# Kernel tuning notes

Hardware: AMD Instinct MI355X
Metric: run time of the kernel (lower is better)

## Reference

```python
import jax, jax.numpy as jnp
import numpy as np

EPS = 1e-8

def _conv(x, w, b=None):
    # NCHW conv, stride 1, SAME padding (k=3, pad=1)
    y = jax.lax.conv_general_dilated(x, w, (1, 1), 'SAME',
                                     dimension_numbers=('NCHW', 'OIHW', 'NCHW'))
    if b is not None:
        y = y + b[None, :, None, None]
    return y

def setup_inputs() -> dict:
    key = jax.random.key(0)
    ks = jax.random.split(key, 6)
    B, C, H, W = 512, 1024, 8, 8
    return {
        'x': jax.random.normal(ks[0], (B, C, H, W), jnp.float32),
        'w1_1': jax.random.normal(ks[1], (1, 1, 3, 3), jnp.float32) * 0.1,
        'w5': jax.random.normal(ks[2], (4, 2, 3, 3), jnp.float32) * 0.1,
        'b5': jax.random.normal(ks[3], (4,), jnp.float32) * 0.1,
        'w6': jax.random.normal(ks[4], (1, 4, 3, 3), jnp.float32) * 0.1,
        'b6': jax.random.normal(ks[5], (1,), jnp.float32) * 0.1,
    }

def reference(x, w1_1, w5, b5, w6, b6):
    B, C, H, W = x.shape  # H == W == 8 by module construction
    m = jnp.max(x, axis=1, keepdims=True)  # [B,1,H,W] channel max
    # 2x2 non-overlapping windows, torch unfold layout -> [B,1,(H/2)*(W/2),4]
    win = m.reshape(B, 1, H // 2, 2, W // 2, 2)
    win = win.transpose(0, 1, 2, 4, 3, 5).reshape(B, 1, (H // 2) * (W // 2), 4)
    # probabilistic pooling: clean inf/nan/negatives, sample per window
    winc = jnp.where(jnp.isinf(win) | jnp.isnan(win) | (win < 0), EPS, win)
    skey = jax.random.key(1)
    idx = jax.random.categorical(skey, winc, axis=-1)  # softmax(winc) multinomial
    mo2 = jnp.take_along_axis(winc, idx[..., None], axis=-1)[..., 0]
    mo2 = mo2.reshape(B, 1, H // 2, W // 2)
    # adaptive max/avg pool (4,4) on 8x8 == 2x2 pooling, reuse windows
    mo3 = win.max(axis=-1).reshape(B, 1, H // 2, W // 2)
    ao4 = win.mean(axis=-1).reshape(B, 1, H // 2, W // 2)
    out2 = 0.1 * mo2 + 0.6 * mo3 + 0.3 * ao4
    out2 = _conv(out2, w1_1)  # bias-free 1->1 conv
    out2 = jax.image.resize(out2, (B, 1, H, W), method='bilinear')  # align_corners=False
    out1 = jnp.concatenate([m, out2], axis=1)  # [B,2,H,W]
    gate = jax.nn.sigmoid(_conv(jax.nn.relu(_conv(out1, w5, b5)), w6, b6))  # [B,1,H,W]
    return jax.nn.relu(x * gate)
```

## Files before the change

### kernel.cpp

```cpp
#include <hip/hip_runtime.h>
#include <math.h>

#define C_DIM 1024
#define HW 64
#define F4B 16384
#define EPSV 1e-8f
#define TINYF 1.17549435e-38f

typedef float f32x4_t __attribute__((ext_vector_type(4)));

__device__ __forceinline__ void threefry2x32_01(unsigned x0, unsigned x1,
                                                unsigned& o0, unsigned& o1) {
    const unsigned ks0 = 0u, ks1 = 1u, ks2 = 0x1BD11BDBu;
    x0 += ks0; x1 += ks1;
#define TF_R(r) { x0 += x1; x1 = (x1 << (r)) | (x1 >> (32 - (r))); x1 ^= x0; }
    TF_R(13) TF_R(15) TF_R(26) TF_R(6)
    x0 += ks1; x1 += ks2 + 1u;
    TF_R(17) TF_R(29) TF_R(16) TF_R(24)
    x0 += ks2; x1 += ks0 + 2u;
    TF_R(13) TF_R(15) TF_R(26) TF_R(6)
    x0 += ks0; x1 += ks1 + 3u;
    TF_R(17) TF_R(29) TF_R(16) TF_R(24)
    x0 += ks1; x1 += ks2 + 4u;
    TF_R(13) TF_R(15) TF_R(26) TF_R(6)
    x0 += ks2; x1 += ks0 + 5u;
#undef TF_R
    o0 = x0; o1 = x1;
}

__device__ __forceinline__ unsigned jax_random_bits(unsigned n) {
    unsigned o0, o1;
    threefry2x32_01(0u, n, o0, o1);
    return o0 ^ o1;
}

__device__ __forceinline__ float gumbel01(unsigned n) {
    unsigned bits = jax_random_bits(n);
    float f = __uint_as_float(0x3F800000u | (bits >> 9)) - 1.0f;
    float u = fmaxf(TINYF, f + TINYF);
    return -logf(-logf(u));
}

__device__ __forceinline__ bool bad_val(float v) {
    return ((__float_as_uint(v) & 0x7F800000u) == 0x7F800000u) || (v < 0.0f);
}

__global__ __launch_bounds__(256) void sa_maxpart_kernel(
    const float* __restrict__ x,
    float* __restrict__ part)
{
    const int bid = blockIdx.x;
    const int t = threadIdx.x;
    const int b = bid >> 2, q = bid & 3;

    const float4* __restrict__ xq =
        (const float4*)x + (size_t)b * F4B + (size_t)q * 4096;

    float4 pm = make_float4(-INFINITY, -INFINITY, -INFINITY, -INFINITY);
#pragma unroll
    for (int i = 0; i < 16; ++i) {
        float4 v = xq[t + 256 * i];
        pm.x = fmaxf(pm.x, v.x); pm.y = fmaxf(pm.y, v.y);
        pm.z = fmaxf(pm.z, v.z); pm.w = fmaxf(pm.w, v.w);
    }
#pragma unroll
    for (int off = 16; off <= 32; off <<= 1) {
        pm.x = fmaxf(pm.x, __shfl_xor(pm.x, off, 64));
        pm.y = fmaxf(pm.y, __shfl_xor(pm.y, off, 64));
        pm.z = fmaxf(pm.z, __shfl_xor(pm.z, off, 64));
        pm.w = fmaxf(pm.w, __shfl_xor(pm.w, off, 64));
    }
    __shared__ float4 red[4 * 16];
    const int wv = t >> 6, lane = t & 63;
    if (lane < 16) red[wv * 16 + lane] = pm;
    __syncthreads();
    if (t < 16) {
        float4 a = red[t];
#pragma unroll
        for (int w = 1; w < 4; ++w) {
            float4 o = red[w * 16 + t];
            a.x = fmaxf(a.x, o.x); a.y = fmaxf(a.y, o.y);
            a.z = fmaxf(a.z, o.z); a.w = fmaxf(a.w, o.w);
        }
        float* dst = part + ((size_t)b * 4 + q) * 64 + t * 4;
        dst[0] = a.x; dst[1] = a.y; dst[2] = a.z; dst[3] = a.w;
    }
}

__global__ __launch_bounds__(64) void sa_middle_kernel(
    const float* __restrict__ part,
    const float* __restrict__ w11,
    const float* __restrict__ w5,
    const float* __restrict__ b5,
    const float* __restrict__ w6,
    const float* __restrict__ b6,
    float* __restrict__ gate)
{
    const int b = blockIdx.x;
    const int t = threadIdx.x;

    __shared__ float sm[64], sa16[16], sb16[16], so2[64], shid[4 * 64];

    const float* pb = part + (size_t)b * 256;
    float m = fmaxf(fmaxf(pb[t], pb[64 + t]), fmaxf(pb[128 + t], pb[192 + t]));
    sm[t] = m;
    const float sgum = gumbel01((unsigned)(b * 64 + t));
    __builtin_amdgcn_wave_barrier();

    {
        int w = t >> 2, j = t & 3;
        int hh = 2 * (w >> 2) + (j >> 1), ww = 2 * (w & 3) + (j & 1);
        float v = sm[hh * 8 + ww];
        float wc = bad_val(v) ? EPSV : v;
        float s = wc + sgum;
        int bi = j;
        float bwc = wc;
        float mx = v;
        float ssum = v;
#pragma unroll
        for (int mk = 1; mk <= 2; mk <<= 1) {
            float s2   = __shfl_xor(s, mk, 64);
            int   bi2  = __shfl_xor(bi, mk, 64);
            float bwc2 = __shfl_xor(bwc, mk, 64);
            float mx2  = __shfl_xor(mx, mk, 64);
            float ss2  = __shfl_xor(ssum, mk, 64);
            bool take = (s2 > s) || (s2 == s && bi2 < bi);
            if (take) { s = s2; bi = bi2; bwc = bwc2; }
            mx = fmaxf(mx, mx2);
            ssum += ss2;
        }
        if (j == 0) sa16[w] = 0.1f * bwc + 0.6f * mx + 0.3f * (ssum * 0.25f);
    }
    __builtin_amdgcn_wave_barrier();

    if (t < 16) {
        int i = t >> 2, j = t & 3;
        float acc = 0.0f;
#pragma unroll
        for (int dy = -1; dy <= 1; ++dy) {
            int yy = i + dy;
            if (yy < 0 || yy > 3) continue;
#pragma unroll
            for (int dx = -1; dx <= 1; ++dx) {
                int xx = j + dx;
                if (xx < 0 || xx > 3) continue;
                acc += sa16[yy * 4 + xx] * w11[(dy + 1) * 3 + (dx + 1)];
            }
        }
        sb16[t] = acc;
    }
    __builtin_amdgcn_wave_barrier();

    {
        int y = t >> 3, xx2 = t & 7;
        float sy = (y + 0.5f) * 0.5f - 0.5f;
        float sx = (xx2 + 0.5f) * 0.5f - 0.5f;
        float fy = fminf(fmaxf(sy, 0.0f), 3.0f);
        float fx = fminf(fmaxf(sx, 0.0f), 3.0f);
        int iy0 = (int)floorf(fy); int iy1 = min(iy0 + 1, 3); float ry = fy - (float)iy0;
        int ix0 = (int)floorf(fx); int ix1 = min(ix0 + 1, 3); float rx = fx - (float)ix0;
        float v00 = sb16[iy0 * 4 + ix0], v01 = sb16[iy0 * 4 + ix1];
        float v10 = sb16[iy1 * 4 + ix0], v11 = sb16[iy1 * 4 + ix1];
        float top = v00 * (1.0f - rx) + v01 * rx;
        float bot = v10 * (1.0f - rx) + v11 * rx;
        so2[t] = top * (1.0f - ry) + bot * ry;
    }
    __builtin_amdgcn_wave_barrier();

    {
        int y = t >> 3, x2 = t & 7;
        float a0 = b5[0], a1 = b5[1], a2 = b5[2], a3 = b5[3];
#pragma unroll
        for (int dy = -1; dy <= 1; ++dy) {
            int yy = y + dy;
            if (yy < 0 || yy > 7) continue;
#pragma unroll
            for (int dx = -1; dx <= 1; ++dx) {
                int xx = x2 + dx;
                if (xx < 0 || xx > 7) continue;
                float i0 = sm[yy * 8 + xx];
                float i1 = so2[yy * 8 + xx];
                int kk = (dy + 1) * 3 + (dx + 1);
                a0 += i0 * w5[0 * 18 + kk] + i1 * w5[0 * 18 + 9 + kk];
                a1 += i0 * w5[1 * 18 + kk] + i1 * w5[1 * 18 + 9 + kk];
                a2 += i0 * w5[2 * 18 + kk] + i1 * w5[2 * 18 + 9 + kk];
                a3 += i0 * w5[3 * 18 + kk] + i1 * w5[3 * 18 + 9 + kk];
            }
        }
        shid[0 * 64 + t] = fmaxf(a0, 0.0f);
        shid[1 * 64 + t] = fmaxf(a1, 0.0f);
        shid[2 * 64 + t] = fmaxf(a2, 0.0f);
        shid[3 * 64 + t] = fmaxf(a3, 0.0f);
    }
    __builtin_amdgcn_wave_barrier();

    {
        int y = t >> 3, x2 = t & 7;
        float acc = b6[0];
#pragma unroll
        for (int dy = -1; dy <= 1; ++dy) {
            int yy = y + dy;
            if (yy < 0 || yy > 7) continue;
#pragma unroll
            for (int dx = -1; dx <= 1; ++dx) {
                int xx = x2 + dx;
                if (xx < 0 || xx > 7) continue;
                int kk = (dy + 1) * 3 + (dx + 1);
                int p = yy * 8 + xx;
                acc += shid[0 * 64 + p] * w6[0 + kk]
                     + shid[1 * 64 + p] * w6[9 + kk]
                     + shid[2 * 64 + p] * w6[18 + kk]
                     + shid[3 * 64 + p] * w6[27 + kk];
            }
        }
        gate[(size_t)b * 64 + t] = 1.0f / (1.0f + expf(-acc));
    }
}

__global__ __launch_bounds__(256) void sa_apply_kernel(
    const float* __restrict__ x,
    const float* __restrict__ gate,
    float* __restrict__ out)
{
    const int bid = blockIdx.x;
    const int t = threadIdx.x;
    const int b = bid >> 2;
    const size_t base = (size_t)bid * 4096;

    const float4* __restrict__ x4 = (const float4*)x;
    float4* __restrict__ o4 = (float4*)out;

    const float4 gv = ((const float4*)(gate + (size_t)b * 64))[t & 15];

#pragma unroll
    for (int i = 0; i < 16; ++i) {
        size_t idx = base + t + 256 * i;
        float4 v = x4[idx];
        f32x4_t o;
        o.x = fmaxf(v.x * gv.x, 0.0f);
        o.y = fmaxf(v.y * gv.y, 0.0f);
        o.z = fmaxf(v.z * gv.z, 0.0f);
        o.w = fmaxf(v.w * gv.w, 0.0f);
        __builtin_nontemporal_store(o, (f32x4_t*)&o4[idx]);
    }
}

extern "C" void kernel_launch(void* const* d_in, const int* in_sizes, int n_in,
                              void* d_out, int out_size, void* d_ws, size_t ws_size,
                              hipStream_t stream) {
    const float* x   = (const float*)d_in[0];
    const float* w11 = (const float*)d_in[1];
    const float* w5  = (const float*)d_in[2];
    const float* b5  = (const float*)d_in[3];
    const float* w6  = (const float*)d_in[4];
    const float* b6  = (const float*)d_in[5];
    float* out  = (float*)d_out;

    int B = in_sizes[0] / (C_DIM * HW);
    float* gate = (float*)d_ws;
    float* part = (float*)d_ws + (size_t)B * 64;

    sa_maxpart_kernel<<<dim3(B * 4), dim3(256), 0, stream>>>(x, part);
    sa_middle_kernel<<<dim3(B), dim3(64), 0, stream>>>(part, w11, w5, b5, w6, b6, gate);
    sa_apply_kernel<<<dim3(B * 4), dim3(256), 0, stream>>>(x, gate, out);
}
```

Before: 262.4 us.

## Fuse three kernels into one cooperative kernel with grid-wide syncs

Replaces the separate max-reduction, middle gate, and apply launches with one cooperative kernel of 2*B blocks. Each block handles two channel quarters, and grid.sync separates the three phases. This is meant to remove launch gaps between kernels and to let the second pass over x hit in cache. The cost is two grid-wide barriers, a cap on grid size from the cooperative-launch occupancy limit, and only B of the 2B blocks doing the tiny middle work.

```diff
diff --git a/kernel.cpp b/kernel.cpp
--- a/kernel.cpp
+++ b/kernel.cpp
@@ -1,5 +1,8 @@
 #include <hip/hip_runtime.h>
+#include <hip/hip_cooperative_groups.h>
 #include <math.h>
+
+namespace cg = cooperative_groups;
 
 #define C_DIM 1024
 #define HW 64
@@ -45,203 +48,202 @@
     return ((__float_as_uint(v) & 0x7F800000u) == 0x7F800000u) || (v < 0.0f);
 }
 
-__global__ __launch_bounds__(256) void sa_maxpart_kernel(
+__global__ __launch_bounds__(256, 4) void sa_coop_kernel(
     const float* __restrict__ x,
-    float* __restrict__ part)
-{
-    const int bid = blockIdx.x;
-    const int t = threadIdx.x;
-    const int b = bid >> 2, q = bid & 3;
-
-    const float4* __restrict__ xq =
-        (const float4*)x + (size_t)b * F4B + (size_t)q * 4096;
-
-    float4 pm = make_float4(-INFINITY, -INFINITY, -INFINITY, -INFINITY);
-#pragma unroll
-    for (int i = 0; i < 16; ++i) {
-        float4 v = xq[t + 256 * i];
-        pm.x = fmaxf(pm.x, v.x); pm.y = fmaxf(pm.y, v.y);
-        pm.z = fmaxf(pm.z, v.z); pm.w = fmaxf(pm.w, v.w);
-    }
-#pragma unroll
-    for (int off = 16; off <= 32; off <<= 1) {
-        pm.x = fmaxf(pm.x, __shfl_xor(pm.x, off, 64));
-        pm.y = fmaxf(pm.y, __shfl_xor(pm.y, off, 64));
-        pm.z = fmaxf(pm.z, __shfl_xor(pm.z, off, 64));
-        pm.w = fmaxf(pm.w, __shfl_xor(pm.w, off, 64));
-    }
-    __shared__ float4 red[4 * 16];
-    const int wv = t >> 6, lane = t & 63;
-    if (lane < 16) red[wv * 16 + lane] = pm;
-    __syncthreads();
-    if (t < 16) {
-        float4 a = red[t];
-#pragma unroll
-        for (int w = 1; w < 4; ++w) {
-            float4 o = red[w * 16 + t];
-            a.x = fmaxf(a.x, o.x); a.y = fmaxf(a.y, o.y);
-            a.z = fmaxf(a.z, o.z); a.w = fmaxf(a.w, o.w);
-        }
-        float* dst = part + ((size_t)b * 4 + q) * 64 + t * 4;
-        dst[0] = a.x; dst[1] = a.y; dst[2] = a.z; dst[3] = a.w;
-    }
-}
-
-__global__ __launch_bounds__(64) void sa_middle_kernel(
-    const float* __restrict__ part,
     const float* __restrict__ w11,
     const float* __restrict__ w5,
     const float* __restrict__ b5,
     const float* __restrict__ w6,
     const float* __restrict__ b6,
-    float* __restrict__ gate)
+    float* __restrict__ out,
+    float* __restrict__ part,
+    float* __restrict__ gate,
+    int B)
 {
-    const int b = blockIdx.x;
-    const int t = threadIdx.x;
-
-    __shared__ float sm[64], sa16[16], sb16[16], so2[64], shid[4 * 64];
-
-    const float* pb = part + (size_t)b * 256;
-    float m = fmaxf(fmaxf(pb[t], pb[64 + t]), fmaxf(pb[128 + t], pb[192 + t]));
-    sm[t] = m;
-    const float sgum = gumbel01((unsigned)(b * 64 + t));
-    __builtin_amdgcn_wave_barrier();
-
-    {
-        int w = t >> 2, j = t & 3;
-        int hh = 2 * (w >> 2) + (j >> 1), ww = 2 * (w & 3) + (j & 1);
-        float v = sm[hh * 8 + ww];
-        float wc = bad_val(v) ? EPSV : v;
-        float s = wc + sgum;
-        int bi = j;
-        float bwc = wc;
-        float mx = v;
-        float ssum = v;
-#pragma unroll
-        for (int mk = 1; mk <= 2; mk <<= 1) {
-            float s2   = __shfl_xor(s, mk, 64);
-            int   bi2  = __shfl_xor(bi, mk, 64);
-            float bwc2 = __shfl_xor(bwc, mk, 64);
-            float mx2  = __shfl_xor(mx, mk, 64);
-            float ss2  = __shfl_xor(ssum, mk, 64);
-            bool take = (s2 > s) || (s2 == s && bi2 < bi);
-            if (take) { s = s2; bi = bi2; bwc = bwc2; }
-            mx = fmaxf(mx, mx2);
-            ssum += ss2;
-        }
-        if (j == 0) sa16[w] = 0.1f * bwc + 0.6f * mx + 0.3f * (ssum * 0.25f);
-    }
-    __builtin_amdgcn_wave_barrier();
-
-    if (t < 16) {
-        int i = t >> 2, j = t & 3;
-        float acc = 0.0f;
-#pragma unroll
-        for (int dy = -1; dy <= 1; ++dy) {
-            int yy = i + dy;
-            if (yy < 0 || yy > 3) continue;
-#pragma unroll
-            for (int dx = -1; dx <= 1; ++dx) {
-                int xx = j + dx;
-                if (xx < 0 || xx > 3) continue;
-                acc += sa16[yy * 4 + xx] * w11[(dy + 1) * 3 + (dx + 1)];
-            }
-        }
-        sb16[t] = acc;
-    }
-    __builtin_amdgcn_wave_barrier();
-
-    {
-        int y = t >> 3, xx2 = t & 7;
-        float sy = (y + 0.5f) * 0.5f - 0.5f;
-        float sx = (xx2 + 0.5f) * 0.5f - 0.5f;
-        float fy = fminf(fmaxf(sy, 0.0f), 3.0f);
-        float fx = fminf(fmaxf(sx, 0.0f), 3.0f);
-        int iy0 = (int)floorf(fy); int iy1 = min(iy0 + 1, 3); float ry = fy - (float)iy0;
-        int ix0 = (int)floorf(fx); int ix1 = min(ix0 + 1, 3); float rx = fx - (float)ix0;
-        float v00 = sb16[iy0 * 4 + ix0], v01 = sb16[iy0 * 4 + ix1];
-        float v10 = sb16[iy1 * 4 + ix0], v11 = sb16[iy1 * 4 + ix1];
-        float top = v00 * (1.0f - rx) + v01 * rx;
-        float bot = v10 * (1.0f - rx) + v11 * rx;
-        so2[t] = top * (1.0f - ry) + bot * ry;
-    }
-    __builtin_amdgcn_wave_barrier();
-
-    {
-        int y = t >> 3, x2 = t & 7;
-        float a0 = b5[0], a1 = b5[1], a2 = b5[2], a3 = b5[3];
-#pragma unroll
-        for (int dy = -1; dy <= 1; ++dy) {
-            int yy = y + dy;
-            if (yy < 0 || yy > 7) continue;
-#pragma unroll
-            for (int dx = -1; dx <= 1; ++dx) {
-                int xx = x2 + dx;
-                if (xx < 0 || xx > 7) continue;
-                float i0 = sm[yy * 8 + xx];
-                float i1 = so2[yy * 8 + xx];
-                int kk = (dy + 1) * 3 + (dx + 1);
-                a0 += i0 * w5[0 * 18 + kk] + i1 * w5[0 * 18 + 9 + kk];
-                a1 += i0 * w5[1 * 18 + kk] + i1 * w5[1 * 18 + 9 + kk];
-                a2 += i0 * w5[2 * 18 + kk] + i1 * w5[2 * 18 + 9 + kk];
-                a3 += i0 * w5[3 * 18 + kk] + i1 * w5[3 * 18 + 9 + kk];
-            }
-        }
-        shid[0 * 64 + t] = fmaxf(a0, 0.0f);
-        shid[1 * 64 + t] = fmaxf(a1, 0.0f);
-        shid[2 * 64 + t] = fmaxf(a2, 0.0f);
-        shid[3 * 64 + t] = fmaxf(a3, 0.0f);
-    }
-    __builtin_amdgcn_wave_barrier();
-
-    {
-        int y = t >> 3, x2 = t & 7;
-        float acc = b6[0];
-#pragma unroll
-        for (int dy = -1; dy <= 1; ++dy) {
-            int yy = y + dy;
-            if (yy < 0 || yy > 7) continue;
-#pragma unroll
-            for (int dx = -1; dx <= 1; ++dx) {
-                int xx = x2 + dx;
-                if (xx < 0 || xx > 7) continue;
-                int kk = (dy + 1) * 3 + (dx + 1);
-                int p = yy * 8 + xx;
-                acc += shid[0 * 64 + p] * w6[0 + kk]
-                     + shid[1 * 64 + p] * w6[9 + kk]
-                     + shid[2 * 64 + p] * w6[18 + kk]
-                     + shid[3 * 64 + p] * w6[27 + kk];
-            }
-        }
-        gate[(size_t)b * 64 + t] = 1.0f / (1.0f + expf(-acc));
-    }
-}
-
-__global__ __launch_bounds__(256) void sa_apply_kernel(
-    const float* __restrict__ x,
-    const float* __restrict__ gate,
-    float* __restrict__ out)
-{
+    cg::grid_group grid = cg::this_grid();
     const int bid = blockIdx.x;
     const int t = threadIdx.x;
-    const int b = bid >> 2;
-    const size_t base = (size_t)bid * 4096;
-
+    const int nblk = gridDim.x;
     const float4* __restrict__ x4 = (const float4*)x;
     float4* __restrict__ o4 = (float4*)out;
 
-    const float4 gv = ((const float4*)(gate + (size_t)b * 64))[t & 15];
-
-#pragma unroll
-    for (int i = 0; i < 16; ++i) {
-        size_t idx = base + t + 256 * i;
-        float4 v = x4[idx];
-        f32x4_t o;
-        o.x = fmaxf(v.x * gv.x, 0.0f);
-        o.y = fmaxf(v.y * gv.y, 0.0f);
-        o.z = fmaxf(v.z * gv.z, 0.0f);
-        o.w = fmaxf(v.w * gv.w, 0.0f);
-        __builtin_nontemporal_store(o, (f32x4_t*)&o4[idx]);
+    __shared__ float4 red[2][4 * 16];
+    __shared__ float sm[64], sa16[16], sb16[16], so2[64], shid[4 * 64];
+
+#pragma unroll
+    for (int r = 0; r < 2; ++r) {
+        const int qb = bid + r * nblk;
+        const size_t base = (size_t)qb * 4096;
+        float4 pm = make_float4(-INFINITY, -INFINITY, -INFINITY, -INFINITY);
+#pragma unroll
+        for (int i = 0; i < 16; ++i) {
+            float4 v = x4[base + t + 256 * i];
+            pm.x = fmaxf(pm.x, v.x); pm.y = fmaxf(pm.y, v.y);
+            pm.z = fmaxf(pm.z, v.z); pm.w = fmaxf(pm.w, v.w);
+        }
+#pragma unroll
+        for (int off = 16; off <= 32; off <<= 1) {
+            pm.x = fmaxf(pm.x, __shfl_xor(pm.x, off, 64));
+            pm.y = fmaxf(pm.y, __shfl_xor(pm.y, off, 64));
+            pm.z = fmaxf(pm.z, __shfl_xor(pm.z, off, 64));
+            pm.w = fmaxf(pm.w, __shfl_xor(pm.w, off, 64));
+        }
+        const int wv = t >> 6, lane = t & 63;
+        if (lane < 16) red[r][wv * 16 + lane] = pm;
+    }
+    __syncthreads();
+    if (t < 16) {
+#pragma unroll
+        for (int r = 0; r < 2; ++r) {
+            float4 a = red[r][t];
+#pragma unroll
+            for (int w = 1; w < 4; ++w) {
+                float4 o = red[r][w * 16 + t];
+                a.x = fmaxf(a.x, o.x); a.y = fmaxf(a.y, o.y);
+                a.z = fmaxf(a.z, o.z); a.w = fmaxf(a.w, o.w);
+            }
+            float* dst = part + (size_t)(bid + r * nblk) * 64 + t * 4;
+            dst[0] = a.x; dst[1] = a.y; dst[2] = a.z; dst[3] = a.w;
+        }
+    }
+    grid.sync();
+
+    if (bid < B && t < 64) {
+        const int b = bid;
+        const float* pb = part + (size_t)b * 256;
+        float m = fmaxf(fmaxf(pb[t], pb[64 + t]), fmaxf(pb[128 + t], pb[192 + t]));
+        sm[t] = m;
+        const float sgum = gumbel01((unsigned)(b * 64 + t));
+        __builtin_amdgcn_wave_barrier();
+
+        {
+            int w = t >> 2, j = t & 3;
+            int hh = 2 * (w >> 2) + (j >> 1), ww = 2 * (w & 3) + (j & 1);
+            float v = sm[hh * 8 + ww];
+            float wc = bad_val(v) ? EPSV : v;
+            float s = wc + sgum;
+            int bi = j;
+            float bwc = wc;
+            float mx = v;
+            float ssum = v;
+#pragma unroll
+            for (int mk = 1; mk <= 2; mk <<= 1) {
+                float s2   = __shfl_xor(s, mk, 64);
+                int   bi2  = __shfl_xor(bi, mk, 64);
+                float bwc2 = __shfl_xor(bwc, mk, 64);
+                float mx2  = __shfl_xor(mx, mk, 64);
+                float ss2  = __shfl_xor(ssum, mk, 64);
+                bool take = (s2 > s) || (s2 == s && bi2 < bi);
+                if (take) { s = s2; bi = bi2; bwc = bwc2; }
+                mx = fmaxf(mx, mx2);
+                ssum += ss2;
+            }
+            if (j == 0) sa16[w] = 0.1f * bwc + 0.6f * mx + 0.3f * (ssum * 0.25f);
+        }
+        __builtin_amdgcn_wave_barrier();
+
+        if (t < 16) {
+            int i = t >> 2, j = t & 3;
+            float acc = 0.0f;
+#pragma unroll
+            for (int dy = -1; dy <= 1; ++dy) {
+                int yy = i + dy;
+                if (yy < 0 || yy > 3) continue;
+#pragma unroll
+                for (int dx = -1; dx <= 1; ++dx) {
+                    int xx = j + dx;
+                    if (xx < 0 || xx > 3) continue;
+                    acc += sa16[yy * 4 + xx] * w11[(dy + 1) * 3 + (dx + 1)];
+                }
+            }
+            sb16[t] = acc;
+        }
+        __builtin_amdgcn_wave_barrier();
+
+        {
+            int y = t >> 3, xx2 = t & 7;
+            float sy = (y + 0.5f) * 0.5f - 0.5f;
+            float sx = (xx2 + 0.5f) * 0.5f - 0.5f;
+            float fy = fminf(fmaxf(sy, 0.0f), 3.0f);
+            float fx = fminf(fmaxf(sx, 0.0f), 3.0f);
+            int iy0 = (int)floorf(fy); int iy1 = min(iy0 + 1, 3); float ry = fy - (float)iy0;
+            int ix0 = (int)floorf(fx); int ix1 = min(ix0 + 1, 3); float rx = fx - (float)ix0;
+            float v00 = sb16[iy0 * 4 + ix0], v01 = sb16[iy0 * 4 + ix1];
+            float v10 = sb16[iy1 * 4 + ix0], v11 = sb16[iy1 * 4 + ix1];
+            float top = v00 * (1.0f - rx) + v01 * rx;
+            float bot = v10 * (1.0f - rx) + v11 * rx;
+            so2[t] = top * (1.0f - ry) + bot * ry;
+        }
+        __builtin_amdgcn_wave_barrier();
+
+        {
+            int y = t >> 3, x2 = t & 7;
+            float a0 = b5[0], a1 = b5[1], a2 = b5[2], a3 = b5[3];
+#pragma unroll
+            for (int dy = -1; dy <= 1; ++dy) {
+                int yy = y + dy;
+                if (yy < 0 || yy > 7) continue;
+#pragma unroll
+                for (int dx = -1; dx <= 1; ++dx) {
+                    int xx = x2 + dx;
+                    if (xx < 0 || xx > 7) continue;
+                    float i0 = sm[yy * 8 + xx];
+                    float i1 = so2[yy * 8 + xx];
+                    int kk = (dy + 1) * 3 + (dx + 1);
+                    a0 += i0 * w5[0 * 18 + kk] + i1 * w5[0 * 18 + 9 + kk];
+                    a1 += i0 * w5[1 * 18 + kk] + i1 * w5[1 * 18 + 9 + kk];
+                    a2 += i0 * w5[2 * 18 + kk] + i1 * w5[2 * 18 + 9 + kk];
+                    a3 += i0 * w5[3 * 18 + kk] + i1 * w5[3 * 18 + 9 + kk];
+                }
+            }
+            shid[0 * 64 + t] = fmaxf(a0, 0.0f);
+            shid[1 * 64 + t] = fmaxf(a1, 0.0f);
+            shid[2 * 64 + t] = fmaxf(a2, 0.0f);
+            shid[3 * 64 + t] = fmaxf(a3, 0.0f);
+        }
+        __builtin_amdgcn_wave_barrier();
+
+        {
+            int y = t >> 3, x2 = t & 7;
+            float acc = b6[0];
+#pragma unroll
+            for (int dy = -1; dy <= 1; ++dy) {
+                int yy = y + dy;
+                if (yy < 0 || yy > 7) continue;
+#pragma unroll
+                for (int dx = -1; dx <= 1; ++dx) {
+                    int xx = x2 + dx;
+                    if (xx < 0 || xx > 7) continue;
+                    int kk = (dy + 1) * 3 + (dx + 1);
+                    int p = yy * 8 + xx;
+                    acc += shid[0 * 64 + p] * w6[0 + kk]
+                         + shid[1 * 64 + p] * w6[9 + kk]
+                         + shid[2 * 64 + p] * w6[18 + kk]
+                         + shid[3 * 64 + p] * w6[27 + kk];
+                }
+            }
+            gate[(size_t)b * 64 + t] = 1.0f / (1.0f + expf(-acc));
+        }
+    }
+    grid.sync();
+
+#pragma unroll
+    for (int r = 0; r < 2; ++r) {
+        const int qb = bid + r * nblk;
+        const int b = qb >> 2;
+        const size_t base = (size_t)qb * 4096;
+        const float4 gv = ((const float4*)(gate + (size_t)b * 64))[t & 15];
+#pragma unroll
+        for (int i = 0; i < 16; ++i) {
+            size_t idx = base + t + 256 * i;
+            float4 v = x4[idx];
+            f32x4_t o;
+            o.x = fmaxf(v.x * gv.x, 0.0f);
+            o.y = fmaxf(v.y * gv.y, 0.0f);
+            o.z = fmaxf(v.z * gv.z, 0.0f);
+            o.w = fmaxf(v.w * gv.w, 0.0f);
+            __builtin_nontemporal_store(o, (f32x4_t*)&o4[idx]);
+        }
     }
 }
 
@@ -260,7 +262,10 @@
     float* gate = (float*)d_ws;
     float* part = (float*)d_ws + (size_t)B * 64;
 
-    sa_maxpart_kernel<<<dim3(B * 4), dim3(256), 0, stream>>>(x, part);
-    sa_middle_kernel<<<dim3(B), dim3(64), 0, stream>>>(part, w11, w5, b5, w6, b6, gate);
-    sa_apply_kernel<<<dim3(B * 4), dim3(256), 0, stream>>>(x, gate, out);
-}
+    int nblk = B * 2;
+    void* args[] = { (void*)&x, (void*)&w11, (void*)&w5, (void*)&b5,
+                     (void*)&w6, (void*)&b6, (void*)&out,
+                     (void*)&part, (void*)&gate, (void*)&B };
+    hipLaunchCooperativeKernel((const void*)sa_coop_kernel,
+                               dim3(nblk), dim3(256), args, 0, stream);
+}
```

After: 471.5 us. 1.8x slower.

## Fuse max, gate and apply kernels into one pass with per-batch spin sync

Applied to the files above, without the earlier changes.

Merges the three kernels into a single kernel. The four blocks of each batch element sync through an atomic counter, then each block computes the 64-element gate locally in shared memory and applies it to its own quarter of x. The intent is to drop two launches and the gate round trip through memory, and to re-read x while it is still cached. The cost is a memset launch, spin-waiting, and the assumption that all four blocks of a batch are co-resident. Without that residency the kernel could deadlock.

```diff
diff --git a/kernel.cpp b/kernel.cpp
--- a/kernel.cpp
+++ b/kernel.cpp
@@ -4,10 +4,15 @@
 #define C_DIM 1024
 #define HW 64
 #define F4B 16384
+#define QF4 4096
 #define EPSV 1e-8f
 #define TINYF 1.17549435e-38f
 
 typedef float f32x4_t __attribute__((ext_vector_type(4)));
+
+__device__ __forceinline__ float devload(const float* p) {
+    return __hip_atomic_load(p, __ATOMIC_RELAXED, __HIP_MEMORY_SCOPE_AGENT);
+}
 
 __device__ __forceinline__ void threefry2x32_01(unsigned x0, unsigned x1,
                                                 unsigned& o0, unsigned& o1) {
@@ -45,16 +50,27 @@
     return ((__float_as_uint(v) & 0x7F800000u) == 0x7F800000u) || (v < 0.0f);
 }
 
-__global__ __launch_bounds__(256) void sa_maxpart_kernel(
+__global__ __launch_bounds__(256, 8) void sa_onepass_kernel(
     const float* __restrict__ x,
+    const float* __restrict__ w11,
+    const float* __restrict__ w5,
+    const float* __restrict__ b5,
+    const float* __restrict__ w6,
+    const float* __restrict__ b6,
+    float* __restrict__ out,
+    int* __restrict__ cnt,
     float* __restrict__ part)
 {
     const int bid = blockIdx.x;
     const int t = threadIdx.x;
     const int b = bid >> 2, q = bid & 3;
 
-    const float4* __restrict__ xq =
-        (const float4*)x + (size_t)b * F4B + (size_t)q * 4096;
+    const float4* __restrict__ xq = (const float4*)x + (size_t)b * F4B + (size_t)q * QF4;
+    float4* __restrict__ oq = (float4*)out + (size_t)b * F4B + (size_t)q * QF4;
+
+    __shared__ float4 red[4 * 16];
+    __shared__ float sm[64], sa16[16], sb16[16], so2[64], shid[4 * 64];
+    __shared__ __align__(16) float sgate[64];
 
     float4 pm = make_float4(-INFINITY, -INFINITY, -INFINITY, -INFINITY);
 #pragma unroll
@@ -70,7 +86,6 @@
         pm.z = fmaxf(pm.z, __shfl_xor(pm.z, off, 64));
         pm.w = fmaxf(pm.w, __shfl_xor(pm.w, off, 64));
     }
-    __shared__ float4 red[4 * 16];
     const int wv = t >> 6, lane = t & 63;
     if (lane < 16) red[wv * 16 + lane] = pm;
     __syncthreads();
@@ -85,163 +100,147 @@
         float* dst = part + ((size_t)b * 4 + q) * 64 + t * 4;
         dst[0] = a.x; dst[1] = a.y; dst[2] = a.z; dst[3] = a.w;
     }
-}
-
-__global__ __launch_bounds__(64) void sa_middle_kernel(
-    const float* __restrict__ part,
-    const float* __restrict__ w11,
-    const float* __restrict__ w5,
-    const float* __restrict__ b5,
-    const float* __restrict__ w6,
-    const float* __restrict__ b6,
-    float* __restrict__ gate)
-{
-    const int b = blockIdx.x;
-    const int t = threadIdx.x;
-
-    __shared__ float sm[64], sa16[16], sb16[16], so2[64], shid[4 * 64];
-
-    const float* pb = part + (size_t)b * 256;
-    float m = fmaxf(fmaxf(pb[t], pb[64 + t]), fmaxf(pb[128 + t], pb[192 + t]));
-    sm[t] = m;
-    const float sgum = gumbel01((unsigned)(b * 64 + t));
-    __builtin_amdgcn_wave_barrier();
-
-    {
-        int w = t >> 2, j = t & 3;
-        int hh = 2 * (w >> 2) + (j >> 1), ww = 2 * (w & 3) + (j & 1);
-        float v = sm[hh * 8 + ww];
-        float wc = bad_val(v) ? EPSV : v;
-        float s = wc + sgum;
-        int bi = j;
-        float bwc = wc;
-        float mx = v;
-        float ssum = v;
-#pragma unroll
-        for (int mk = 1; mk <= 2; mk <<= 1) {
-            float s2   = __shfl_xor(s, mk, 64);
-            int   bi2  = __shfl_xor(bi, mk, 64);
-            float bwc2 = __shfl_xor(bwc, mk, 64);
-            float mx2  = __shfl_xor(mx, mk, 64);
-            float ss2  = __shfl_xor(ssum, mk, 64);
-            bool take = (s2 > s) || (s2 == s && bi2 < bi);
-            if (take) { s = s2; bi = bi2; bwc = bwc2; }
-            mx = fmaxf(mx, mx2);
-            ssum += ss2;
-        }
-        if (j == 0) sa16[w] = 0.1f * bwc + 0.6f * mx + 0.3f * (ssum * 0.25f);
-    }
-    __builtin_amdgcn_wave_barrier();
-
-    if (t < 16) {
-        int i = t >> 2, j = t & 3;
-        float acc = 0.0f;
-#pragma unroll
-        for (int dy = -1; dy <= 1; ++dy) {
-            int yy = i + dy;
-            if (yy < 0 || yy > 3) continue;
-#pragma unroll
-            for (int dx = -1; dx <= 1; ++dx) {
-                int xx = j + dx;
-                if (xx < 0 || xx > 3) continue;
-                acc += sa16[yy * 4 + xx] * w11[(dy + 1) * 3 + (dx + 1)];
-            }
-        }
-        sb16[t] = acc;
-    }
-    __builtin_amdgcn_wave_barrier();
-
-    {
-        int y = t >> 3, xx2 = t & 7;
-        float sy = (y + 0.5f) * 0.5f - 0.5f;
-        float sx = (xx2 + 0.5f) * 0.5f - 0.5f;
-        float fy = fminf(fmaxf(sy, 0.0f), 3.0f);
-        float fx = fminf(fmaxf(sx, 0.0f), 3.0f);
-        int iy0 = (int)floorf(fy); int iy1 = min(iy0 + 1, 3); float ry = fy - (float)iy0;
-        int ix0 = (int)floorf(fx); int ix1 = min(ix0 + 1, 3); float rx = fx - (float)ix0;
-        float v00 = sb16[iy0 * 4 + ix0], v01 = sb16[iy0 * 4 + ix1];
-        float v10 = sb16[iy1 * 4 + ix0], v11 = sb16[iy1 * 4 + ix1];
-        float top = v00 * (1.0f - rx) + v01 * rx;
-        float bot = v10 * (1.0f - rx) + v11 * rx;
-        so2[t] = top * (1.0f - ry) + bot * ry;
-    }
-    __builtin_amdgcn_wave_barrier();
-
-    {
-        int y = t >> 3, x2 = t & 7;
-        float a0 = b5[0], a1 = b5[1], a2 = b5[2], a3 = b5[3];
-#pragma unroll
-        for (int dy = -1; dy <= 1; ++dy) {
-            int yy = y + dy;
-            if (yy < 0 || yy > 7) continue;
-#pragma unroll
-            for (int dx = -1; dx <= 1; ++dx) {
-                int xx = x2 + dx;
-                if (xx < 0 || xx > 7) continue;
-                float i0 = sm[yy * 8 + xx];
-                float i1 = so2[yy * 8 + xx];
-                int kk = (dy + 1) * 3 + (dx + 1);
-                a0 += i0 * w5[0 * 18 + kk] + i1 * w5[0 * 18 + 9 + kk];
-                a1 += i0 * w5[1 * 18 + kk] + i1 * w5[1 * 18 + 9 + kk];
-                a2 += i0 * w5[2 * 18 + kk] + i1 * w5[2 * 18 + 9 + kk];
-                a3 += i0 * w5[3 * 18 + kk] + i1 * w5[3 * 18 + 9 + kk];
-            }
-        }
-        shid[0 * 64 + t] = fmaxf(a0, 0.0f);
-        shid[1 * 64 + t] = fmaxf(a1, 0.0f);
-        shid[2 * 64 + t] = fmaxf(a2, 0.0f);
-        shid[3 * 64 + t] = fmaxf(a3, 0.0f);
-    }
-    __builtin_amdgcn_wave_barrier();
-
-    {
-        int y = t >> 3, x2 = t & 7;
-        float acc = b6[0];
-#pragma unroll
-        for (int dy = -1; dy <= 1; ++dy) {
-            int yy = y + dy;
-            if (yy < 0 || yy > 7) continue;
-#pragma unroll
-            for (int dx = -1; dx <= 1; ++dx) {
-                int xx = x2 + dx;
-                if (xx < 0 || xx > 7) continue;
-                int kk = (dy + 1) * 3 + (dx + 1);
-                int p = yy * 8 + xx;
-                acc += shid[0 * 64 + p] * w6[0 + kk]
-                     + shid[1 * 64 + p] * w6[9 + kk]
-                     + shid[2 * 64 + p] * w6[18 + kk]
-                     + shid[3 * 64 + p] * w6[27 + kk];
-            }
-        }
-        gate[(size_t)b * 64 + t] = 1.0f / (1.0f + expf(-acc));
-    }
-}
-
-__global__ __launch_bounds__(256) void sa_apply_kernel(
-    const float* __restrict__ x,
-    const float* __restrict__ gate,
-    float* __restrict__ out)
-{
-    const int bid = blockIdx.x;
-    const int t = threadIdx.x;
-    const int b = bid >> 2;
-    const size_t base = (size_t)bid * 4096;
-
-    const float4* __restrict__ x4 = (const float4*)x;
-    float4* __restrict__ o4 = (float4*)out;
-
-    const float4 gv = ((const float4*)(gate + (size_t)b * 64))[t & 15];
-
+    __syncthreads();
+
+    if (t == 0) {
+        __threadfence();
+        __hip_atomic_fetch_add(&cnt[b], 1, __ATOMIC_RELEASE,
+                               __HIP_MEMORY_SCOPE_AGENT);
+        while (__hip_atomic_load(&cnt[b], __ATOMIC_ACQUIRE,
+                                 __HIP_MEMORY_SCOPE_AGENT) < 4)
+            __builtin_amdgcn_s_sleep(8);
+    }
+    __syncthreads();
+
+    if (t < 64) {
+        const float* pb = part + (size_t)b * 256;
+        float m = fmaxf(fmaxf(devload(pb + t),       devload(pb + 64 + t)),
+                        fmaxf(devload(pb + 128 + t), devload(pb + 192 + t)));
+        sm[t] = m;
+        const float sgum = gumbel01((unsigned)(b * 64 + t));
+        __builtin_amdgcn_wave_barrier();
+
+        {
+            int w = t >> 2, j = t & 3;
+            int hh = 2 * (w >> 2) + (j >> 1), ww = 2 * (w & 3) + (j & 1);
+            float v = sm[hh * 8 + ww];
+            float wc = bad_val(v) ? EPSV : v;
+            float s = wc + sgum;
+            int bi = j;
+            float bwc = wc;
+            float mx = v;
+            float ssum = v;
+#pragma unroll
+            for (int mk = 1; mk <= 2; mk <<= 1) {
+                float s2   = __shfl_xor(s, mk, 64);
+                int   bi2  = __shfl_xor(bi, mk, 64);
+                float bwc2 = __shfl_xor(bwc, mk, 64);
+                float mx2  = __shfl_xor(mx, mk, 64);
+                float ss2  = __shfl_xor(ssum, mk, 64);
+                bool take = (s2 > s) || (s2 == s && bi2 < bi);
+                if (take) { s = s2; bi = bi2; bwc = bwc2; }
+                mx = fmaxf(mx, mx2);
+                ssum += ss2;
+            }
+            if (j == 0) sa16[w] = 0.1f * bwc + 0.6f * mx + 0.3f * (ssum * 0.25f);
+        }
+        __builtin_amdgcn_wave_barrier();
+
+        if (t < 16) {
+            int i = t >> 2, j = t & 3;
+            float acc = 0.0f;
+#pragma unroll
+            for (int dy = -1; dy <= 1; ++dy) {
+                int yy = i + dy;
+                if (yy < 0 || yy > 3) continue;
+#pragma unroll
+                for (int dx = -1; dx <= 1; ++dx) {
+                    int xx = j + dx;
+                    if (xx < 0 || xx > 3) continue;
+                    acc += sa16[yy * 4 + xx] * w11[(dy + 1) * 3 + (dx + 1)];
+                }
+            }
+            sb16[t] = acc;
+        }
+        __builtin_amdgcn_wave_barrier();
+
+        {
+            int y = t >> 3, xx2 = t & 7;
+            float sy = (y + 0.5f) * 0.5f - 0.5f;
+            float sx = (xx2 + 0.5f) * 0.5f - 0.5f;
+            float fy = fminf(fmaxf(sy, 0.0f), 3.0f);
+            float fx = fminf(fmaxf(sx, 0.0f), 3.0f);
+            int iy0 = (int)floorf(fy); int iy1 = min(iy0 + 1, 3); float ry = fy - (float)iy0;
+            int ix0 = (int)floorf(fx); int ix1 = min(ix0 + 1, 3); float rx = fx - (float)ix0;
+            float v00 = sb16[iy0 * 4 + ix0], v01 = sb16[iy0 * 4 + ix1];
+            float v10 = sb16[iy1 * 4 + ix0], v11 = sb16[iy1 * 4 + ix1];
+            float top = v00 * (1.0f - rx) + v01 * rx;
+            float bot = v10 * (1.0f - rx) + v11 * rx;
+            so2[t] = top * (1.0f - ry) + bot * ry;
+        }
+        __builtin_amdgcn_wave_barrier();
+
+        {
+            int y = t >> 3, x2 = t & 7;
+            float a0 = b5[0], a1 = b5[1], a2 = b5[2], a3 = b5[3];
+#pragma unroll
+            for (int dy = -1; dy <= 1; ++dy) {
+                int yy = y + dy;
+                if (yy < 0 || yy > 7) continue;
+#pragma unroll
+                for (int dx = -1; dx <= 1; ++dx) {
+                    int xx = x2 + dx;
+                    if (xx < 0 || xx > 7) continue;
+                    float i0 = sm[yy * 8 + xx];
+                    float i1 = so2[yy * 8 + xx];
+                    int kk = (dy + 1) * 3 + (dx + 1);
+                    a0 += i0 * w5[0 * 18 + kk] + i1 * w5[0 * 18 + 9 + kk];
+                    a1 += i0 * w5[1 * 18 + kk] + i1 * w5[1 * 18 + 9 + kk];
+                    a2 += i0 * w5[2 * 18 + kk] + i1 * w5[2 * 18 + 9 + kk];
+                    a3 += i0 * w5[3 * 18 + kk] + i1 * w5[3 * 18 + 9 + kk];
+                }
+            }
+            shid[0 * 64 + t] = fmaxf(a0, 0.0f);
+            shid[1 * 64 + t] = fmaxf(a1, 0.0f);
+            shid[2 * 64 + t] = fmaxf(a2, 0.0f);
+            shid[3 * 64 + t] = fmaxf(a3, 0.0f);
+        }
+        __builtin_amdgcn_wave_barrier();
+
+        {
+            int y = t >> 3, x2 = t & 7;
+            float acc = b6[0];
+#pragma unroll
+            for (int dy = -1; dy <= 1; ++dy) {
+                int yy = y + dy;
+                if (yy < 0 || yy > 7) continue;
+#pragma unroll
+                for (int dx = -1; dx <= 1; ++dx) {
+                    int xx = x2 + dx;
+                    if (xx < 0 || xx > 7) continue;
+                    int kk = (dy + 1) * 3 + (dx + 1);
+                    int p = yy * 8 + xx;
+                    acc += shid[0 * 64 + p] * w6[0 + kk]
+                         + shid[1 * 64 + p] * w6[9 + kk]
+                         + shid[2 * 64 + p] * w6[18 + kk]
+                         + shid[3 * 64 + p] * w6[27 + kk];
+                }
+            }
+            sgate[t] = 1.0f / (1.0f + expf(-acc));
+        }
+    }
+    __syncthreads();
+
+    const float4 gv = ((const float4*)sgate)[t & 15];
 #pragma unroll
     for (int i = 0; i < 16; ++i) {
-        size_t idx = base + t + 256 * i;
-        float4 v = x4[idx];
+        float4 v = xq[t + 256 * i];
         f32x4_t o;
         o.x = fmaxf(v.x * gv.x, 0.0f);
         o.y = fmaxf(v.y * gv.y, 0.0f);
         o.z = fmaxf(v.z * gv.z, 0.0f);
         o.w = fmaxf(v.w * gv.w, 0.0f);
-        __builtin_nontemporal_store(o, (f32x4_t*)&o4[idx]);
+        __builtin_nontemporal_store(o, (f32x4_t*)&oq[t + 256 * i]);
     }
 }
 
@@ -257,10 +256,10 @@
     float* out  = (float*)d_out;
 
     int B = in_sizes[0] / (C_DIM * HW);
-    float* gate = (float*)d_ws;
-    float* part = (float*)d_ws + (size_t)B * 64;
-
-    sa_maxpart_kernel<<<dim3(B * 4), dim3(256), 0, stream>>>(x, part);
-    sa_middle_kernel<<<dim3(B), dim3(64), 0, stream>>>(part, w11, w5, b5, w6, b6, gate);
-    sa_apply_kernel<<<dim3(B * 4), dim3(256), 0, stream>>>(x, gate, out);
-}
+    int* cnt = (int*)d_ws;
+    float* part = (float*)d_ws + 512;
+
+    hipMemsetAsync(d_ws, 0, (size_t)B * sizeof(int), stream);
+    sa_onepass_kernel<<<dim3(B * 4), dim3(256), 0, stream>>>(
+        x, w11, w5, b5, w6, b6, out, cnt, part);
+}
```

Result: slower. 463.6 us (+76.7%).
